# Kernel optimization log

Measured on AMD Instinct MI355X. Metric: run time of the kernel, lower is better.

The kernel has to match this reference:

```python
import jax, jax.numpy as jnp
import numpy as np

EPS = 1e-5
NEG_SLOPE = 0.2  # PyG GATConv default leaky_relu slope


def group_norm(x, w, b, groups):
    # x: [N, C] treated as batch of N samples, GroupNorm over channel groups
    N, C = x.shape
    xg = x.reshape(N, groups, C // groups)
    mu = xg.mean(-1, keepdims=True)
    var = ((xg - mu) ** 2).mean(-1, keepdims=True)
    xn = ((xg - mu) / jnp.sqrt(var + EPS)).reshape(N, C)
    return xn * w + b


def gat_conv(x, src, dst, W, a_src, a_dst, bias, n_nodes):
    # PyG GATConv, heads=1, concat=False, self-loops already appended to src/dst
    h = x @ W.T                                    # [N, C]
    alpha_src = h @ a_src                          # [N]
    alpha_dst = h @ a_dst                          # [N]
    e = jax.nn.leaky_relu(alpha_src[src] + alpha_dst[dst], NEG_SLOPE)  # [E]
    # segment softmax over edges grouped by destination node
    m = jax.ops.segment_max(e, dst, num_segments=n_nodes)
    ex = jnp.exp(e - m[dst])
    s = jax.ops.segment_sum(ex, dst, num_segments=n_nodes)
    alpha = ex / (s[dst] + 1e-16)                  # [E]
    out = jax.ops.segment_sum(h[src] * alpha[:, None], dst, num_segments=n_nodes)
    return out + bias


def setup_inputs() -> dict:
    key = jax.random.key(0)
    ks = jax.random.split(key, 32)
    N, E = 40000, 640000
    C_IN, C_OUT = 256, 512
    H = C_OUT // 2  # 256

    def xavier(k, shape):
        fan_in, fan_out = shape[1], shape[0]
        lim = np.sqrt(6.0 / (fan_in + fan_out))
        return jax.random.uniform(k, shape, jnp.float32, -lim, lim)

    inp = {
        "x": jax.random.normal(ks[0], (N, C_IN), jnp.float32),
        "edge_index": jax.random.randint(ks[1], (2, E), 0, N, jnp.int64),
        # pre_norm (GroupNorm(C_IN//8, C_IN))
        "pre_w": jnp.ones((C_IN,), jnp.float32),
        "pre_b": jnp.zeros((C_IN,), jnp.float32),
        # lin1: C_IN -> H
        "lin1_w": xavier(ks[2], (H, C_IN)),
        "lin1_b": jnp.zeros((H,), jnp.float32),
        "n1_w": jnp.ones((H,), jnp.float32),
        "n1_b": jnp.zeros((H,), jnp.float32),
        # GATConv 1 (H -> H, heads=1)
        "g1_w": xavier(ks[3], (H, H)),
        "g1_asrc": jax.random.normal(ks[4], (H,), jnp.float32) * 0.1,
        "g1_adst": jax.random.normal(ks[5], (H,), jnp.float32) * 0.1,
        "g1_b": jnp.zeros((H,), jnp.float32),
        "n2_w": jnp.ones((H,), jnp.float32),
        "n2_b": jnp.zeros((H,), jnp.float32),
        # GATConv 2
        "g2_w": xavier(ks[6], (H, H)),
        "g2_asrc": jax.random.normal(ks[7], (H,), jnp.float32) * 0.1,
        "g2_adst": jax.random.normal(ks[8], (H,), jnp.float32) * 0.1,
        "g2_b": jnp.zeros((H,), jnp.float32),
        "n3_w": jnp.ones((H,), jnp.float32),
        "n3_b": jnp.zeros((H,), jnp.float32),
        # lin2: H -> C_OUT
        "lin2_w": xavier(ks[9], (C_OUT, H)),
        "lin2_b": jnp.zeros((C_OUT,), jnp.float32),
        # skip_conv: C_IN -> C_OUT (in != out, so skip is applied)
        "skip_w": xavier(ks[10], (C_OUT, C_IN)),
        "skip_b": jnp.zeros((C_OUT,), jnp.float32),
    }
    return inp


def reference(x, edge_index, pre_w, pre_b, lin1_w, lin1_b, n1_w, n1_b,
              g1_w, g1_asrc, g1_adst, g1_b, n2_w, n2_b,
              g2_w, g2_asrc, g2_adst, g2_b, n3_w, n3_b,
              lin2_w, lin2_b, skip_w, skip_b):
    N, C_IN = x.shape
    H = lin1_w.shape[0]
    # add self loops (PyG GATConv default add_self_loops=True)
    loops = jnp.arange(N, dtype=edge_index.dtype)
    src = jnp.concatenate([edge_index[0], loops])
    dst = jnp.concatenate([edge_index[1], loops])

    y = jax.nn.elu(group_norm(x, pre_w, pre_b, C_IN // 8))
    y = y @ lin1_w.T + lin1_b
    y = jax.nn.elu(group_norm(y, n1_w, n1_b, H // 8))
    y = gat_conv(y, src, dst, g1_w, g1_asrc, g1_adst, g1_b, N)
    y = jax.nn.elu(group_norm(y, n2_w, n2_b, H // 8))
    y = gat_conv(y, src, dst, g2_w, g2_asrc, g2_adst, g2_b, N)
    y = jax.nn.elu(group_norm(y, n3_w, n3_b, H // 8))
    y = y @ lin2_w.T + lin2_b
    x_skip = x @ skip_w.T + skip_b  # in_channels != out_channels
    return x_skip + y
```

## Files before the change

### kernel.cpp

```cpp
#include <hip/hip_runtime.h>
#include <hip/hip_bf16.h>


typedef __bf16 bf16x8 __attribute__((ext_vector_type(8)));
typedef float floatx4 __attribute__((ext_vector_type(4)));
typedef float floatx2 __attribute__((ext_vector_type(2)));

__device__ __forceinline__ __hip_bfloat16 f2b(float f) { return __float2bfloat16(f); }
__device__ __forceinline__ float bits2f(unsigned u) { return __uint_as_float(u << 16); }

__device__ __forceinline__ void gl_lds16(const __hip_bfloat16* g, __hip_bfloat16* l) {
  __builtin_amdgcn_global_load_lds(
      (const __attribute__((address_space(1))) void*)g,
      (__attribute__((address_space(3))) void*)l, 16, 0, 0);
}

__device__ __forceinline__ bf16x8 cvt8(const float* p) {
  float4 a = *(const float4*)p, b = *(const float4*)(p + 4);
  bf16x8 r;
  r[0] = (__bf16)a.x; r[1] = (__bf16)a.y; r[2] = (__bf16)a.z; r[3] = (__bf16)a.w;
  r[4] = (__bf16)b.x; r[5] = (__bf16)b.y; r[6] = (__bf16)b.z; r[7] = (__bf16)b.w;
  return r;
}

__global__ __launch_bounds__(256) void conv_w_k(
    const float* __restrict__ s0, const float* __restrict__ s1,
    const float* __restrict__ s2, const float* __restrict__ s3,
    const float* __restrict__ s4, __hip_bfloat16* __restrict__ d) {
  int i = (blockIdx.x * 256 + threadIdx.x) * 4;
  if (i >= 458752) return;
  const float* s; int off;
  if      (i < 65536)  { s = s0; off = 0; }
  else if (i < 131072) { s = s1; off = 65536; }
  else if (i < 196608) { s = s2; off = 131072; }
  else if (i < 327680) { s = s3; off = 196608; }
  else                 { s = s4; off = 327680; }
  float4 v = *(const float4*)(s + (i - off));
  union { ushort4 u; __hip_bfloat16 h[4]; } st;
  st.h[0] = f2b(v.x); st.h[1] = f2b(v.y); st.h[2] = f2b(v.z); st.h[3] = f2b(v.w);
  *(ushort4*)(d + i) = st.u;
}

__global__ __launch_bounds__(256) void gn_elu_k(
    const float* __restrict__ x, const float* __restrict__ w, const float* __restrict__ b,
    __hip_bfloat16* __restrict__ o, __hip_bfloat16* __restrict__ xb, int ng) {
  int g = blockIdx.x * 256 + threadIdx.x;
  if (g >= ng) return;
  int gi = g & 31;
  size_t basei = (size_t)g * 8;
  float4 u0 = *(const float4*)(x + basei), u1 = *(const float4*)(x + basei + 4);
  float f[8] = {u0.x, u0.y, u0.z, u0.w, u1.x, u1.y, u1.z, u1.w};
  if (xb) {
    union { uint4 u; __hip_bfloat16 h[8]; } xs;
#pragma unroll
    for (int i = 0; i < 8; i++) xs.h[i] = f2b(f[i]);
    *(uint4*)(xb + basei) = xs.u;
  }
  float mu = 0.f;
#pragma unroll
  for (int i = 0; i < 8; i++) mu += f[i];
  mu *= 0.125f;
  float var = 0.f;
#pragma unroll
  for (int i = 0; i < 8; i++) { float d = f[i] - mu; var += d * d; }
  float inv = rsqrtf(var * 0.125f + 1e-5f);
  union { uint4 u; __hip_bfloat16 h[8]; } st;
#pragma unroll
  for (int i = 0; i < 8; i++) {
    float vv = (f[i] - mu) * inv * w[gi * 8 + i] + b[gi * 8 + i];
    vv = (vv > 0.f) ? vv : (__expf(vv) - 1.f);
    st.h[i] = f2b(vv);
  }
  *(uint4*)(o + basei) = st.u;
}

template <int MODE>
__global__ __launch_bounds__(256, 3) void gemm_t(
    const __hip_bfloat16* __restrict__ A, const __hip_bfloat16* __restrict__ A2,
    const float* __restrict__ Af32,
    const __hip_bfloat16* __restrict__ W, const __hip_bfloat16* __restrict__ W2,
    const float* __restrict__ bias, const float* __restrict__ bias2,
    const float* __restrict__ gnw, const float* __restrict__ gnb,
    const float* __restrict__ avs, const float* __restrict__ avd,
    __hip_bfloat16* __restrict__ outB, float* __restrict__ outF,
    float* __restrict__ asrc, float* __restrict__ adst, int Nc, int Mreal) {
  const int tid = threadIdx.x;
  const int wn = tid >> 6, lane = tid & 63;
  const int l16 = lane & 15, quad = lane >> 4;
  const int rows0 = blockIdx.y * 64;
  const int col0 = blockIdx.x * 256;
  const int srow = tid >> 2, skc = (tid & 3) * 8;
  __shared__ __align__(16) __hip_bfloat16 sA[2][64 * 32];
  __shared__ __align__(16) __hip_bfloat16 sB[2][256 * 32];
  __shared__ float sRed[2][64][4];
  const int wbase = wn << 9;

  floatx4 acc[4][4];
#pragma unroll
  for (int a = 0; a < 4; ++a)
#pragma unroll
    for (int b = 0; b < 4; ++b) acc[a][b] = (floatx4){0.f, 0.f, 0.f, 0.f};

  const int NK = (MODE >= 2) ? 16 : 8;

  auto stage = [&](int buf, int kt) {
    const int kk = (kt & 7) * 32;
    const bool sec = (MODE >= 2) && (kt >= 8);
    const __hip_bfloat16* Wb = sec ? W2 : W;
    if (!(MODE == 3 && sec)) {
      const __hip_bfloat16* Ab = (MODE == 2 && sec) ? A2 : A;
      gl_lds16(Ab + (size_t)(rows0 + srow) * 256 + kk + skc, &sA[buf][wbase]);
    }
#pragma unroll
    for (int h = 0; h < 4; ++h)
      gl_lds16(Wb + (size_t)(col0 + srow + h * 64) * 256 + kk + skc,
               &sB[buf][wbase + h * 2048]);
  };

  stage(0, 0);
  __syncthreads();

#pragma unroll
  for (int kt = 0; kt < NK; ++kt) {
    const int cur = kt & 1, nxt = cur ^ 1;
    if (kt + 1 < NK) stage(nxt, kt + 1);
    bf16x8 af[4], bfr[4];
    if (MODE == 3 && kt >= 8) {
      const int kk = (kt & 7) * 32;
#pragma unroll
      for (int ri = 0; ri < 4; ++ri) {
        int row = min(rows0 + ri * 16 + l16, Mreal - 1);
        af[ri] = cvt8(Af32 + (size_t)row * 256 + kk + quad * 8);
      }
    } else {
#pragma unroll
      for (int ri = 0; ri < 4; ++ri)
        af[ri] = *(const bf16x8*)(&sA[cur][(ri * 16 + l16) * 32 + quad * 8]);
    }
#pragma unroll
    for (int ci = 0; ci < 4; ++ci)
      bfr[ci] = *(const bf16x8*)(&sB[cur][(wn * 64 + ci * 16 + l16) * 32 + quad * 8]);
#pragma unroll
    for (int ri = 0; ri < 4; ++ri)
#pragma unroll
      for (int ci = 0; ci < 4; ++ci)
        acc[ri][ci] = __builtin_amdgcn_mfma_f32_16x16x32_bf16(af[ri], bfr[ci], acc[ri][ci], 0, 0, 0);
    __syncthreads();
  }

  if (MODE == 0) {
#pragma unroll
    for (int ri = 0; ri < 4; ++ri)
#pragma unroll
      for (int ci = 0; ci < 4; ++ci) {
        int col = col0 + wn * 64 + ci * 16 + l16;
        float bs = bias[col], gw = gnw[col], gb = gnb[col];
#pragma unroll
        for (int i = 0; i < 4; ++i) {
          float v = acc[ri][ci][i] + bs;
          float s = v;
          s += __shfl_xor(s, 1, 64); s += __shfl_xor(s, 2, 64); s += __shfl_xor(s, 4, 64);
          float mu = s * 0.125f, d = v - mu;
          float q = d * d;
          q += __shfl_xor(q, 1, 64); q += __shfl_xor(q, 2, 64); q += __shfl_xor(q, 4, 64);
          float r = d * rsqrtf(q * 0.125f + 1e-5f) * gw + gb;
          r = (r > 0.f) ? r : (__expf(r) - 1.f);
          outB[(size_t)(rows0 + ri * 16 + quad * 4 + i) * 256 + col] = f2b(r);
        }
      }
  } else if (MODE == 1) {
#pragma unroll
    for (int ri = 0; ri < 4; ++ri) {
      float ps[4] = {0.f, 0.f, 0.f, 0.f}, pd[4] = {0.f, 0.f, 0.f, 0.f};
#pragma unroll
      for (int ci = 0; ci < 4; ++ci) {
        int col = col0 + wn * 64 + ci * 16 + l16;
        float wsv = avs[col], wdv = avd[col];
#pragma unroll
        for (int i = 0; i < 4; ++i) {
          float v = acc[ri][ci][i];
          outB[(size_t)(rows0 + ri * 16 + quad * 4 + i) * 256 + col] = f2b(v);
          ps[i] += v * wsv; pd[i] += v * wdv;
        }
      }
#pragma unroll
      for (int i = 0; i < 4; ++i) {
        ps[i] += __shfl_xor(ps[i], 1, 64); ps[i] += __shfl_xor(ps[i], 2, 64);
        ps[i] += __shfl_xor(ps[i], 4, 64); ps[i] += __shfl_xor(ps[i], 8, 64);
        pd[i] += __shfl_xor(pd[i], 1, 64); pd[i] += __shfl_xor(pd[i], 2, 64);
        pd[i] += __shfl_xor(pd[i], 4, 64); pd[i] += __shfl_xor(pd[i], 8, 64);
        if (l16 == 0) {
          int r = ri * 16 + quad * 4 + i;
          sRed[0][r][wn] = ps[i];
          sRed[1][r][wn] = pd[i];
        }
      }
    }
    __syncthreads();
    if (tid < 128) {
      int arr = tid >> 6, r = tid & 63;
      float v = sRed[arr][r][0] + sRed[arr][r][1] + sRed[arr][r][2] + sRed[arr][r][3];
      (arr ? adst : asrc)[rows0 + r] = v;
    }
  } else {
#pragma unroll
    for (int ri = 0; ri < 4; ++ri)
#pragma unroll
      for (int ci = 0; ci < 4; ++ci) {
        int col = col0 + wn * 64 + ci * 16 + l16;
        float bs = bias[col] + bias2[col];
#pragma unroll
        for (int i = 0; i < 4; ++i) {
          int row = rows0 + ri * 16 + quad * 4 + i;
          if (row < Mreal) outF[(size_t)row * Nc + col] = acc[ri][ci][i] + bs;
        }
      }
  }
}

__global__ void zero_k(int* p, int n) {
  int i = blockIdx.x * blockDim.x + threadIdx.x;
  if (i < n) p[i] = 0;
}

__global__ void count_deg_k(const int* __restrict__ ei, int E, int NN, int* __restrict__ counts) {
  int e = blockIdx.x * blockDim.x + threadIdx.x;
  if (e >= E + NN) return;
  int d = (e < E) ? ei[E + e] : (e - E);
  if ((unsigned)d >= (unsigned)NN) d = 0;
  atomicAdd(&counts[d], 1);
}

__global__ __launch_bounds__(1024) void scan_blk_k(const int* __restrict__ counts,
                                                   int* __restrict__ indptr,
                                                   int* __restrict__ bsums, int NN) {
  __shared__ int wsum[16];
  int t = threadIdx.x, idx = blockIdx.x * 1024 + t;
  int lane = t & 63, wid = t >> 6;
  int v = (idx < NN) ? counts[idx] : 0;
  int s = v;
#pragma unroll
  for (int off = 1; off < 64; off <<= 1) {
    int u = __shfl_up(s, off, 64);
    if (lane >= off) s += u;
  }
  if (lane == 63) wsum[wid] = s;
  __syncthreads();
  if (t == 0) {
    int run = 0;
#pragma unroll
    for (int i = 0; i < 16; i++) { int u = wsum[i]; wsum[i] = run; run += u; }
    bsums[blockIdx.x] = run;
  }
  __syncthreads();
  if (idx < NN) indptr[idx] = s - v + wsum[wid];
}

__global__ void scan_top_k(int* bsums, int nb) {
  if (threadIdx.x == 0) {
    int run = 0;
    for (int i = 0; i < nb; i++) { int t = bsums[i]; bsums[i] = run; run += t; }
  }
}

__global__ __launch_bounds__(1024) void scan_add_k(int* __restrict__ indptr, int* __restrict__ fill,
                                                   const int* __restrict__ bsums, int NN, int ET) {
  int idx = blockIdx.x * 1024 + threadIdx.x;
  if (idx < NN) {
    int v = indptr[idx] + bsums[blockIdx.x];
    indptr[idx] = v; fill[idx] = v;
  }
  if (idx == 0) indptr[NN] = ET;
}

__global__ void fill_csr_k(const int* __restrict__ ei, int E, int NN,
                           int* __restrict__ fill, int* __restrict__ csr, int ET) {
  int e = blockIdx.x * blockDim.x + threadIdx.x;
  if (e >= E + NN) return;
  int s, d;
  if (e < E) { s = ei[e]; d = ei[E + e]; } else { s = e - E; d = e - E; }
  if ((unsigned)d >= (unsigned)NN) d = 0;
  if ((unsigned)s >= (unsigned)NN) s = 0;
  int slot = atomicAdd(&fill[d], 1);
  if ((unsigned)slot < (unsigned)ET) csr[slot] = s;
}

__global__ __launch_bounds__(256) void gat_agg_gn_k(
    const __hip_bfloat16* __restrict__ h, const float* __restrict__ asrc,
    const float* __restrict__ adst, const int* __restrict__ indptr,
    const int* __restrict__ csr, const float* __restrict__ gbias,
    const float* __restrict__ gnw, const float* __restrict__ gnb,
    __hip_bfloat16* __restrict__ outp, int NN, int ET) {
  __shared__ __align__(16) unsigned long long sew[4][64];
  const int wid = threadIdx.x >> 6;
  const int n = blockIdx.x * 4 + wid;
  if (n >= NN) return;
  const int lane = threadIdx.x & 63;
  const int half = lane >> 5, l32 = lane & 31;
  int beg = indptr[n], end = indptr[n + 1];
  beg = max(0, min(beg, ET));
  end = max(beg, min(end, ET));
  const int deg = end - beg;
  const float adn = adst[n];
  floatx2 a0 = {0.f, 0.f}, a1 = {0.f, 0.f}, a2 = {0.f, 0.f}, a3 = {0.f, 0.f};
  float lw = 0.f;

  for (int cb = 0; cb < deg; cb += 64) {
    int j = cb + lane;
    int sid = 0; float w = 0.f;
    if (j < deg) {
      sid = csr[beg + j];
      if ((unsigned)sid >= (unsigned)NN) sid = 0;
      float e = asrc[sid] + adn;
      e = (e > 0.f) ? e : 0.2f * e;
      e = fminf(fmaxf(e, -60.f), 60.f);
      w = __expf(e);
    }
    lw += w;
    sew[wid][lane] = (unsigned)sid | ((unsigned long long)__float_as_uint(w) << 32);
    int cnt = min(64, deg - cb);
    for (int t = 0; t < cnt; t += 8) {
      int s[4]; float wt[4]; uint4 hv[4];
#pragma unroll
      for (int u = 0; u < 4; ++u) {
        unsigned long long pv = sew[wid][t + u * 2 + half];
        s[u] = (int)(unsigned)pv;
        wt[u] = __uint_as_float((unsigned)(pv >> 32));
      }
#pragma unroll
      for (int u = 0; u < 4; ++u)
        hv[u] = *(const uint4*)(h + (size_t)s[u] * 256 + l32 * 8);
#pragma unroll
      for (int u = 0; u < 4; ++u) {
        floatx2 wv = {wt[u], wt[u]};
        floatx2 p;
        p[0] = bits2f(hv[u].x & 0xffffu); p[1] = bits2f(hv[u].x >> 16);
        a0 += wv * p;
        p[0] = bits2f(hv[u].y & 0xffffu); p[1] = bits2f(hv[u].y >> 16);
        a1 += wv * p;
        p[0] = bits2f(hv[u].z & 0xffffu); p[1] = bits2f(hv[u].z >> 16);
        a2 += wv * p;
        p[0] = bits2f(hv[u].w & 0xffffu); p[1] = bits2f(hv[u].w >> 16);
        a3 += wv * p;
      }
    }
  }
  float r8[8] = {a0[0], a0[1], a1[0], a1[1], a2[0], a2[1], a3[0], a3[1]};
#pragma unroll
  for (int i = 0; i < 8; ++i) r8[i] += __shfl_xor(r8[i], 32, 64);
#pragma unroll
  for (int m = 32; m >= 1; m >>= 1) lw += __shfl_xor(lw, m, 64);
  if (half == 0) {
    float inv = 1.f / (lw + 1e-16f);
    int c0 = l32 * 8;
    float v[8], mu = 0.f;
#pragma unroll
    for (int i = 0; i < 8; ++i) { v[i] = r8[i] * inv + gbias[c0 + i]; mu += v[i]; }
    mu *= 0.125f;
    float q = 0.f;
#pragma unroll
    for (int i = 0; i < 8; ++i) { float d = v[i] - mu; q += d * d; }
    float rs = rsqrtf(q * 0.125f + 1e-5f);
    union { uint4 u; __hip_bfloat16 b[8]; } st;
#pragma unroll
    for (int i = 0; i < 8; ++i) {
      float r = (v[i] - mu) * rs * gnw[c0 + i] + gnb[c0 + i];
      r = (r > 0.f) ? r : (__expf(r) - 1.f);
      st.b[i] = f2b(r);
    }
    *(uint4*)(outp + (size_t)n * 256 + c0) = st.u;
  }
}

extern "C" void kernel_launch(void* const* d_in, const int* in_sizes, int n_in,
                              void* d_out, int out_size, void* d_ws, size_t ws_size,
                              hipStream_t stream) {
  const float* x      = (const float*)d_in[0];
  const int*   ei     = (const int*)d_in[1];
  const float* pre_w  = (const float*)d_in[2];
  const float* pre_b  = (const float*)d_in[3];
  const float* lin1_b = (const float*)d_in[5];
  const float* n1_w   = (const float*)d_in[6];
  const float* n1_b   = (const float*)d_in[7];
  const float* g1_as  = (const float*)d_in[9];
  const float* g1_ad  = (const float*)d_in[10];
  const float* g1_b   = (const float*)d_in[11];
  const float* n2_w   = (const float*)d_in[12];
  const float* n2_b   = (const float*)d_in[13];
  const float* g2_as  = (const float*)d_in[15];
  const float* g2_ad  = (const float*)d_in[16];
  const float* g2_b   = (const float*)d_in[17];
  const float* n3_w   = (const float*)d_in[18];
  const float* n3_b   = (const float*)d_in[19];
  const float* lin2_b = (const float*)d_in[21];
  const float* skip_b = (const float*)d_in[23];
  float* out = (float*)d_out;

  const int C_IN  = in_sizes[2];
  const int NN    = in_sizes[0] / C_IN;
  const int E     = in_sizes[1] / 2;
  const int ET    = E + NN;
  const int C_OUT = in_sizes[21];
  const int NP    = (NN + 127) & ~127;

  __hip_bfloat16* D0 = (__hip_bfloat16*)d_out;
  __hip_bfloat16* D1 = D0 + (size_t)NP * 256;

  char* basep = (char*)d_ws;
  size_t o = 0;
  auto alloc = [&](size_t bytes) { size_t r = o; o += (bytes + 255) & ~(size_t)255; return r; };
  __hip_bfloat16* Y      = (__hip_bfloat16*)(basep + alloc((size_t)NP * 256 * 2));
  __hip_bfloat16* Wcat   = (__hip_bfloat16*)(basep + alloc((size_t)458752 * 2));
  float*          asrc   = (float*)(basep + alloc((size_t)NP * 4));
  float*          adst   = (float*)(basep + alloc((size_t)NP * 4));
  int*            indptr = (int*)(basep + alloc((size_t)(NN + 1) * 4));
  int*            counts = (int*)(basep + alloc((size_t)NN * 4));
  int*            fill   = (int*)(basep + alloc((size_t)NN * 4));
  int*            bsums  = (int*)(basep + alloc(256));
  int*            csr    = (int*)(basep + alloc((size_t)ET * 4));
  size_t base_need = o;
  size_t xb_need = ((size_t)NP * 256 * 2 + 255) & ~(size_t)255;
  const bool use_xb = (ws_size >= base_need + xb_need);
  __hip_bfloat16* xb = use_xb ? (__hip_bfloat16*)(basep + alloc(xb_need)) : nullptr;

  __hip_bfloat16* Wlin1 = Wcat;
  __hip_bfloat16* Wg1   = Wcat + 65536;
  __hip_bfloat16* Wg2   = Wcat + 131072;
  __hip_bfloat16* Wlin2 = Wcat + 196608;
  __hip_bfloat16* Wskip = Wcat + 327680;

  dim3 blk(256);
  const int nb = (NN + 1023) / 1024;

  conv_w_k<<<(458752 / 4 + 255) / 256, blk, 0, stream>>>(
      (const float*)d_in[4], (const float*)d_in[8], (const float*)d_in[14],
      (const float*)d_in[20], (const float*)d_in[22], Wcat);
  zero_k<<<(NN + 255) / 256, blk, 0, stream>>>(counts, NN);
  count_deg_k<<<(ET + 255) / 256, blk, 0, stream>>>(ei, E, NN, counts);
  scan_blk_k<<<nb, 1024, 0, stream>>>(counts, indptr, bsums, NN);
  scan_top_k<<<1, 64, 0, stream>>>(bsums, nb);
  scan_add_k<<<nb, 1024, 0, stream>>>(indptr, fill, bsums, NN, ET);
  fill_csr_k<<<(ET + 255) / 256, blk, 0, stream>>>(ei, E, NN, fill, csr, ET);

  gn_elu_k<<<(NN * 32 + 255) / 256, blk, 0, stream>>>(x, pre_w, pre_b, D0, xb, NN * 32);
  gemm_t<0><<<dim3(1, NP / 64), blk, 0, stream>>>(D0, nullptr, nullptr, Wlin1, nullptr,
      lin1_b, nullptr, n1_w, n1_b, nullptr, nullptr, Y, nullptr, nullptr, nullptr, 256, NN);
  gemm_t<1><<<dim3(1, NP / 64), blk, 0, stream>>>(Y, nullptr, nullptr, Wg1, nullptr,
      nullptr, nullptr, nullptr, nullptr, g1_as, g1_ad, D0, nullptr, asrc, adst, 256, NN);
  gat_agg_gn_k<<<NN / 4, blk, 0, stream>>>(D0, asrc, adst, indptr, csr, g1_b, n2_w, n2_b, D1, NN, ET);
  gemm_t<1><<<dim3(1, NP / 64), blk, 0, stream>>>(D1, nullptr, nullptr, Wg2, nullptr,
      nullptr, nullptr, nullptr, nullptr, g2_as, g2_ad, D0, nullptr, asrc, adst, 256, NN);
  gat_agg_gn_k<<<NN / 4, blk, 0, stream>>>(D0, asrc, adst, indptr, csr, g2_b, n3_w, n3_b, Y, NN, ET);
  if (use_xb) {
    gemm_t<2><<<dim3(C_OUT / 256, NP / 64), blk, 0, stream>>>(Y, xb, nullptr, Wlin2, Wskip,
        lin2_b, skip_b, nullptr, nullptr, nullptr, nullptr, nullptr, out, nullptr, nullptr, C_OUT, NN);
  } else {
    gemm_t<3><<<dim3(C_OUT / 256, NP / 64), blk, 0, stream>>>(Y, nullptr, x, Wlin2, Wskip,
        lin2_b, skip_b, nullptr, nullptr, nullptr, nullptr, nullptr, out, nullptr, nullptr, C_OUT, NN);
  }
}
```

Measured before the change: 427.3 us.

## Deepen GEMM LDS pipeline to four buffers with prefetch distance two

Changes the GEMM k-loop from double buffering to a four-slot LDS ring with two tiles in flight. The per-iteration end barrier is replaced by explicit vmcnt waits sized to the outstanding loads plus one s_barrier at the top of each step. sRed now aliases the staging buffer, so a barrier is added before the MODE 1 epilogue. LDS per block grows to 80 KB and launch bounds drop from 3 to 2 blocks per CU, trading occupancy for more memory latency hiding.

```diff
diff --git a/kernel.cpp b/kernel.cpp
--- a/kernel.cpp
+++ b/kernel.cpp
@@ -13,6 +13,17 @@
   __builtin_amdgcn_global_load_lds(
       (const __attribute__((address_space(1))) void*)g,
       (__attribute__((address_space(3))) void*)l, 16, 0, 0);
+}
+
+__device__ __forceinline__ void waitcnt_vm(int n) {
+  switch (n) {
+    case 0:  asm volatile("s_waitcnt vmcnt(0)" ::: "memory"); break;
+    case 4:  asm volatile("s_waitcnt vmcnt(4)" ::: "memory"); break;
+    case 5:  asm volatile("s_waitcnt vmcnt(5)" ::: "memory"); break;
+    case 8:  asm volatile("s_waitcnt vmcnt(8)" ::: "memory"); break;
+    case 9:  asm volatile("s_waitcnt vmcnt(9)" ::: "memory"); break;
+    default: asm volatile("s_waitcnt vmcnt(10)" ::: "memory"); break;
+  }
 }
 
 __device__ __forceinline__ bf16x8 cvt8(const float* p) {
@@ -75,7 +86,7 @@
 }
 
 template <int MODE>
-__global__ __launch_bounds__(256, 3) void gemm_t(
+__global__ __launch_bounds__(256, 2) void gemm_t(
     const __hip_bfloat16* __restrict__ A, const __hip_bfloat16* __restrict__ A2,
     const float* __restrict__ Af32,
     const __hip_bfloat16* __restrict__ W, const __hip_bfloat16* __restrict__ W2,
@@ -90,9 +101,10 @@
   const int rows0 = blockIdx.y * 64;
   const int col0 = blockIdx.x * 256;
   const int srow = tid >> 2, skc = (tid & 3) * 8;
-  __shared__ __align__(16) __hip_bfloat16 sA[2][64 * 32];
-  __shared__ __align__(16) __hip_bfloat16 sB[2][256 * 32];
-  __shared__ float sRed[2][64][4];
+  __shared__ __align__(16) char smem[81920];
+  __hip_bfloat16* sA = (__hip_bfloat16*)smem;
+  __hip_bfloat16* sB = (__hip_bfloat16*)(smem + 16384);
+  float (*sRed)[64][4] = (float (*)[64][4])smem;
   const int wbase = wn << 9;
 
   floatx4 acc[4][4];
@@ -107,23 +119,39 @@
     const int kk = (kt & 7) * 32;
     const bool sec = (MODE >= 2) && (kt >= 8);
     const __hip_bfloat16* Wb = sec ? W2 : W;
+    __hip_bfloat16* sAb = sA + buf * 2048;
+    __hip_bfloat16* sBb = sB + buf * 8192;
     if (!(MODE == 3 && sec)) {
       const __hip_bfloat16* Ab = (MODE == 2 && sec) ? A2 : A;
-      gl_lds16(Ab + (size_t)(rows0 + srow) * 256 + kk + skc, &sA[buf][wbase]);
+      gl_lds16(Ab + (size_t)(rows0 + srow) * 256 + kk + skc, sAb + wbase);
     }
 #pragma unroll
     for (int h = 0; h < 4; ++h)
       gl_lds16(Wb + (size_t)(col0 + srow + h * 64) * 256 + kk + skc,
-               &sB[buf][wbase + h * 2048]);
+               sBb + wbase + h * 2048);
   };
 
   stage(0, 0);
-  __syncthreads();
+  stage(1, 1);
 
 #pragma unroll
   for (int kt = 0; kt < NK; ++kt) {
-    const int cur = kt & 1, nxt = cur ^ 1;
-    if (kt + 1 < NK) stage(nxt, kt + 1);
+    const int cur = kt & 3;
+    if (kt + 2 < NK) stage((kt + 2) & 3, kt + 2);
+    int younger;
+    if (MODE == 3) {
+      if (kt + 2 < NK) younger = (kt + 2 >= 8) ? ((kt + 1 >= 8) ? 8 : 9) : 10;
+      else             younger = (kt + 1 < NK) ? 4 : 0;
+    } else {
+      younger = (kt + 2 < NK) ? 10 : ((kt + 1 < NK) ? 5 : 0);
+    }
+    waitcnt_vm(younger);
+    __builtin_amdgcn_sched_barrier(0);
+    __builtin_amdgcn_s_barrier();
+    __builtin_amdgcn_sched_barrier(0);
+
+    const __hip_bfloat16* sAc = sA + cur * 2048;
+    const __hip_bfloat16* sBc = sB + cur * 8192;
     bf16x8 af[4], bfr[4];
     if (MODE == 3 && kt >= 8) {
       const int kk = (kt & 7) * 32;
@@ -135,17 +163,16 @@
     } else {
 #pragma unroll
       for (int ri = 0; ri < 4; ++ri)
-        af[ri] = *(const bf16x8*)(&sA[cur][(ri * 16 + l16) * 32 + quad * 8]);
+        af[ri] = *(const bf16x8*)(sAc + (ri * 16 + l16) * 32 + quad * 8);
     }
 #pragma unroll
     for (int ci = 0; ci < 4; ++ci)
-      bfr[ci] = *(const bf16x8*)(&sB[cur][(wn * 64 + ci * 16 + l16) * 32 + quad * 8]);
+      bfr[ci] = *(const bf16x8*)(sBc + (wn * 64 + ci * 16 + l16) * 32 + quad * 8);
 #pragma unroll
     for (int ri = 0; ri < 4; ++ri)
 #pragma unroll
       for (int ci = 0; ci < 4; ++ci)
         acc[ri][ci] = __builtin_amdgcn_mfma_f32_16x16x32_bf16(af[ri], bfr[ci], acc[ri][ci], 0, 0, 0);
-    __syncthreads();
   }
 
   if (MODE == 0) {
@@ -169,6 +196,7 @@
         }
       }
   } else if (MODE == 1) {
+    __syncthreads();
 #pragma unroll
     for (int ri = 0; ri < 4; ++ri) {
       float ps[4] = {0.f, 0.f, 0.f, 0.f}, pd[4] = {0.f, 0.f, 0.f, 0.f};
```

Measured after the change: 436.8 us. 1.02x slower.

## Stage full 64x256 A tile into LDS once instead of per-k double buffering

Applied to the files above, without the earlier changes.

The GEMM kernel now loads the whole 64-row by 256-wide A panel into LDS at the start, with 8 async loads per thread, and only double-buffers the weight tiles per k-step. In the dual-GEMM mode the second A operand is reloaded at the midpoint behind an extra barrier. This is meant to issue A loads in bulk and take them off the per-iteration path. In exchange LDS use per block roughly doubles, and launch bounds drop from 3 to 2 blocks per SM, which lowers occupancy.

```diff
diff --git a/kernel.cpp b/kernel.cpp
--- a/kernel.cpp
+++ b/kernel.cpp
@@ -75,7 +75,7 @@
 }
 
 template <int MODE>
-__global__ __launch_bounds__(256, 3) void gemm_t(
+__global__ __launch_bounds__(256, 2) void gemm_t(
     const __hip_bfloat16* __restrict__ A, const __hip_bfloat16* __restrict__ A2,
     const float* __restrict__ Af32,
     const __hip_bfloat16* __restrict__ W, const __hip_bfloat16* __restrict__ W2,
@@ -90,7 +90,7 @@
   const int rows0 = blockIdx.y * 64;
   const int col0 = blockIdx.x * 256;
   const int srow = tid >> 2, skc = (tid & 3) * 8;
-  __shared__ __align__(16) __hip_bfloat16 sA[2][64 * 32];
+  __shared__ __align__(16) __hip_bfloat16 sA[8 * 2048];
   __shared__ __align__(16) __hip_bfloat16 sB[2][256 * 32];
   __shared__ float sRed[2][64][4];
   const int wbase = wn << 9;
@@ -103,27 +103,34 @@
 
   const int NK = (MODE >= 2) ? 16 : 8;
 
-  auto stage = [&](int buf, int kt) {
+  auto stageA = [&](const __hip_bfloat16* Ab) {
+#pragma unroll
+    for (int s = 0; s < 8; ++s)
+      gl_lds16(Ab + (size_t)(rows0 + srow) * 256 + s * 32 + skc, &sA[s * 2048 + wbase]);
+  };
+  auto stageW = [&](int buf, int kt) {
     const int kk = (kt & 7) * 32;
-    const bool sec = (MODE >= 2) && (kt >= 8);
-    const __hip_bfloat16* Wb = sec ? W2 : W;
-    if (!(MODE == 3 && sec)) {
-      const __hip_bfloat16* Ab = (MODE == 2 && sec) ? A2 : A;
-      gl_lds16(Ab + (size_t)(rows0 + srow) * 256 + kk + skc, &sA[buf][wbase]);
-    }
+    const __hip_bfloat16* Wb = ((MODE >= 2) && kt >= 8) ? W2 : W;
 #pragma unroll
     for (int h = 0; h < 4; ++h)
       gl_lds16(Wb + (size_t)(col0 + srow + h * 64) * 256 + kk + skc,
                &sB[buf][wbase + h * 2048]);
   };
 
-  stage(0, 0);
+  stageA(A);
+  stageW(0, 0);
   __syncthreads();
 
 #pragma unroll
   for (int kt = 0; kt < NK; ++kt) {
     const int cur = kt & 1, nxt = cur ^ 1;
-    if (kt + 1 < NK) stage(nxt, kt + 1);
+    if (MODE == 2 && kt == 8) {
+      stageA(A2);
+      if (kt + 1 < NK) stageW(nxt, kt + 1);
+      __syncthreads();
+    } else {
+      if (kt + 1 < NK) stageW(nxt, kt + 1);
+    }
     bf16x8 af[4], bfr[4];
     if (MODE == 3 && kt >= 8) {
       const int kk = (kt & 7) * 32;
@@ -133,9 +140,10 @@
         af[ri] = cvt8(Af32 + (size_t)row * 256 + kk + quad * 8);
       }
     } else {
+      const __hip_bfloat16* sAs = &sA[(kt & 7) * 2048];
 #pragma unroll
       for (int ri = 0; ri < 4; ++ri)
-        af[ri] = *(const bf16x8*)(&sA[cur][(ri * 16 + l16) * 32 + quad * 8]);
+        af[ri] = *(const bf16x8*)(sAs + (ri * 16 + l16) * 32 + quad * 8);
     }
 #pragma unroll
     for (int ci = 0; ci < 4; ++ci)
@@ -431,6 +439,7 @@
 
   dim3 blk(256);
   const int nb = (NN + 1023) / 1024;
+  const int NR = NP / 64;
 
   conv_w_k<<<(458752 / 4 + 255) / 256, blk, 0, stream>>>(
       (const float*)d_in[4], (const float*)d_in[8], (const float*)d_in[14],
@@ -443,19 +452,19 @@
   fill_csr_k<<<(ET + 255) / 256, blk, 0, stream>>>(ei, E, NN, fill, csr, ET);
 
   gn_elu_k<<<(NN * 32 + 255) / 256, blk, 0, stream>>>(x, pre_w, pre_b, D0, xb, NN * 32);
-  gemm_t<0><<<dim3(1, NP / 64), blk, 0, stream>>>(D0, nullptr, nullptr, Wlin1, nullptr,
+  gemm_t<0><<<dim3(1, NR), blk, 0, stream>>>(D0, nullptr, nullptr, Wlin1, nullptr,
       lin1_b, nullptr, n1_w, n1_b, nullptr, nullptr, Y, nullptr, nullptr, nullptr, 256, NN);
-  gemm_t<1><<<dim3(1, NP / 64), blk, 0, stream>>>(Y, nullptr, nullptr, Wg1, nullptr,
+  gemm_t<1><<<dim3(1, NR), blk, 0, stream>>>(Y, nullptr, nullptr, Wg1, nullptr,
       nullptr, nullptr, nullptr, nullptr, g1_as, g1_ad, D0, nullptr, asrc, adst, 256, NN);
   gat_agg_gn_k<<<NN / 4, blk, 0, stream>>>(D0, asrc, adst, indptr, csr, g1_b, n2_w, n2_b, D1, NN, ET);
-  gemm_t<1><<<dim3(1, NP / 64), blk, 0, stream>>>(D1, nullptr, nullptr, Wg2, nullptr,
+  gemm_t<1><<<dim3(1, NR), blk, 0, stream>>>(D1, nullptr, nullptr, Wg2, nullptr,
       nullptr, nullptr, nullptr, nullptr, g2_as, g2_ad, D0, nullptr, asrc, adst, 256, NN);
   gat_agg_gn_k<<<NN / 4, blk, 0, stream>>>(D0, asrc, adst, indptr, csr, g2_b, n3_w, n3_b, Y, NN, ET);
   if (use_xb) {
-    gemm_t<2><<<dim3(C_OUT / 256, NP / 64), blk, 0, stream>>>(Y, xb, nullptr, Wlin2, Wskip,
+    gemm_t<2><<<dim3(C_OUT / 256, NR), blk, 0, stream>>>(Y, xb, nullptr, Wlin2, Wskip,
         lin2_b, skip_b, nullptr, nullptr, nullptr, nullptr, nullptr, out, nullptr, nullptr, C_OUT, NN);
   } else {
-    gemm_t<3><<<dim3(C_OUT / 256, NP / 64), blk, 0, stream>>>(Y, nullptr, x, Wlin2, Wskip,
+    gemm_t<3><<<dim3(C_OUT / 256, NR), blk, 0, stream>>>(Y, nullptr, x, Wlin2, Wskip,
         lin2_b, skip_b, nullptr, nullptr, nullptr, nullptr, nullptr, out, nullptr, nullptr, C_OUT, NN);
   }
 }
```

New measurement: 443.2 us. 1.04x slower.
